# Kernel tuning notes

Hardware: AMD Instinct MI355X
Metric: run time of the kernel (lower is better)

Reference implementation:

```python
import jax, jax.numpy as jnp
import numpy as np

B, S, D, H = 4, 2048, 1024, 16
DK = D // H


def setup_inputs() -> dict:
    key = jax.random.key(0)
    ks = jax.random.split(key, 7)
    s = 1.0 / np.sqrt(D)
    return {
        "q": jax.random.normal(ks[0], (B, S, D), jnp.float32),
        "k": jax.random.normal(ks[1], (B, S, D), jnp.float32),
        "v": jax.random.normal(ks[2], (B, S, D), jnp.float32),
        "Wq": jax.random.normal(ks[3], (D, D), jnp.float32) * s,
        "Wk": jax.random.normal(ks[4], (D, D), jnp.float32) * s,
        "Wv": jax.random.normal(ks[5], (D, D), jnp.float32) * s,
        "Wo": jax.random.normal(ks[6], (D, D), jnp.float32) * s,
    }


def _split(x):
    # [B,S,D] -> [B,H,S,DK]
    return x.reshape(B, S, H, DK).transpose(0, 2, 1, 3)


def reference(q, k, v, Wq, Wk, Wv, Wo):
    # Linear projections (nn.Linear with bias=False: x @ W^T)
    qh = _split(q @ Wq.T)
    kh = _split(k @ Wk.T)
    vh = _split(v @ Wv.T)
    scale = 1.0 / jnp.sqrt(jnp.asarray(DK, qh.dtype))
    # attention scores [B,H,S,S]
    attn = jnp.einsum("bhqd,bhkd->bhqk", qh, kh) * scale
    # causal mask: disallow k > q
    causal = jnp.tril(jnp.ones((S, S), dtype=bool))
    attn = jnp.where(causal[None, None], attn, -jnp.inf)
    attn = jax.nn.softmax(attn, axis=-1)  # dropout p=0.0 -> identity
    out = jnp.einsum("bhqk,bhkd->bhqd", attn, vh)
    # combine heads [B,H,S,DK] -> [B,S,D]
    out = out.transpose(0, 2, 1, 3).reshape(B, S, D)
    return out @ Wo.T
```

## Files before the change

kernel.cpp:

```cpp
#include <hip/hip_runtime.h>
#include <math.h>
#include <stdint.h>

#define B_  4
#define S_  2048
#define D_  1024
#define H_  16
#define DK_ 64
#define NR_ (B_ * S_)

typedef _Float16 half8  __attribute__((ext_vector_type(8)));
typedef _Float16 half4  __attribute__((ext_vector_type(4)));
typedef float    floatx4 __attribute__((ext_vector_type(4)));

__global__ __launch_bounds__(256)
void split_f32(const float* __restrict__ src, _Float16* __restrict__ hi,
               _Float16* __restrict__ lo, int n8) {
    const int i = blockIdx.x * 256 + threadIdx.x;
    if (i >= n8) return;
    const float4* s4 = (const float4*)src;
    float4 a = s4[2 * i];
    float4 b = s4[2 * i + 1];
    float f[8] = {a.x, a.y, a.z, a.w, b.x, b.y, b.z, b.w};
    union { half8 v; _Float16 h[8]; } H, L;
    #pragma unroll
    for (int j = 0; j < 8; ++j) {
        _Float16 h = (_Float16)f[j];
        H.h[j] = h;
        L.h[j] = (_Float16)(f[j] - (float)h);
    }
    *(half8*)(hi + (size_t)i * 8) = H.v;
    *(half8*)(lo + (size_t)i * 8) = L.v;
}

__global__ __launch_bounds__(256)
void split_w4(const float* __restrict__ w0, const float* __restrict__ w1,
              const float* __restrict__ w2, const float* __restrict__ w3,
              _Float16* __restrict__ wbase, int n8) {
    const int i = blockIdx.x * 256 + threadIdx.x;
    if (i >= n8) return;
    const float* src = (blockIdx.y == 0) ? w0 : (blockIdx.y == 1) ? w1 :
                       (blockIdx.y == 2) ? w2 : w3;
    _Float16* hi = wbase + (size_t)blockIdx.y * 2 * ((size_t)D_ * D_);
    _Float16* lo = hi + (size_t)D_ * D_;
    const float4* s4 = (const float4*)src;
    float4 a = s4[2 * i];
    float4 b = s4[2 * i + 1];
    float f[8] = {a.x, a.y, a.z, a.w, b.x, b.y, b.z, b.w};
    union { half8 v; _Float16 h[8]; } H, L;
    #pragma unroll
    for (int j = 0; j < 8; ++j) {
        _Float16 h = (_Float16)f[j];
        H.h[j] = h;
        L.h[j] = (_Float16)(f[j] - (float)h);
    }
    *(half8*)(hi + (size_t)i * 8) = H.v;
    *(half8*)(lo + (size_t)i * 8) = L.v;
}

#define GBN 128
#define GBM 128
#define GBK 32
#define LDH 40

__global__ __launch_bounds__(256, 3)
void gemm_xwt_mfma(const _Float16* __restrict__ Xh, const _Float16* __restrict__ Xl,
                   const _Float16* __restrict__ Wh, const _Float16* __restrict__ Wl,
                   void* __restrict__ out0, int mode) {
    __shared__ __align__(16) _Float16 Whi[GBM][LDH];
    __shared__ __align__(16) _Float16 Wlo[GBM][LDH];
    const int K = D_;

    const int tid  = threadIdx.x;
    const int wave = tid >> 6;
    const int lane = tid & 63;
    const int row16 = lane & 15;
    const int quad  = lane >> 4;
    const int n0 = blockIdx.x * GBN;
    const int m0 = blockIdx.y * GBM;

    const int wrow = tid >> 1;
    const int wc   = (tid & 1) << 4;

    const _Float16* aHb = Xh + (size_t)(n0 + wave * 32 + row16) * K + quad * 8;
    const _Float16* aLb = Xl + (size_t)(n0 + wave * 32 + row16) * K + quad * 8;

    floatx4 acc[2][8];
    const floatx4 zero4 = {0.f, 0.f, 0.f, 0.f};
    #pragma unroll
    for (int i = 0; i < 2; ++i)
        #pragma unroll
        for (int j = 0; j < 8; ++j) acc[i][j] = zero4;

    half8 pa_h0, pa_h1, pa_l0, pa_l1;
    uint4 wh0, wh1, wl0, wl1;
    auto load_regs = [&](int k0) {
        pa_h0 = *(const half8*)(aHb + k0);
        pa_h1 = *(const half8*)(aHb + (size_t)16 * K + k0);
        pa_l0 = *(const half8*)(aLb + k0);
        pa_l1 = *(const half8*)(aLb + (size_t)16 * K + k0);
        const _Float16* pwh = Wh + (size_t)(m0 + wrow) * K + k0 + wc;
        const _Float16* pwl = Wl + (size_t)(m0 + wrow) * K + k0 + wc;
        wh0 = *(const uint4*)pwh;
        wh1 = *(const uint4*)(pwh + 8);
        wl0 = *(const uint4*)pwl;
        wl1 = *(const uint4*)(pwl + 8);
    };

    load_regs(0);
    for (int k0 = 0; k0 < K; k0 += GBK) {
        half8 a_hi[2] = {pa_h0, pa_h1};
        half8 a_lo[2] = {pa_l0, pa_l1};
        __syncthreads();
        *(uint4*)&Whi[wrow][wc]     = wh0;
        *(uint4*)&Whi[wrow][wc + 8] = wh1;
        *(uint4*)&Wlo[wrow][wc]     = wl0;
        *(uint4*)&Wlo[wrow][wc + 8] = wl1;
        __syncthreads();
        if (k0 + GBK < K) load_regs(k0 + GBK);

        #pragma unroll
        for (int mj = 0; mj < 8; ++mj) {
            const int r = mj * 16 + row16;
            half8 b_hi = *(const half8*)&Whi[r][quad * 8];
            half8 b_lo = *(const half8*)&Wlo[r][quad * 8];
            #pragma unroll
            for (int ni = 0; ni < 2; ++ni) {
                acc[ni][mj] = __builtin_amdgcn_mfma_f32_16x16x32_f16(
                    a_hi[ni], b_hi, acc[ni][mj], 0, 0, 0);
                acc[ni][mj] = __builtin_amdgcn_mfma_f32_16x16x32_f16(
                    a_hi[ni], b_lo, acc[ni][mj], 0, 0, 0);
                acc[ni][mj] = __builtin_amdgcn_mfma_f32_16x16x32_f16(
                    a_lo[ni], b_hi, acc[ni][mj], 0, 0, 0);
            }
        }
    }

    #pragma unroll
    for (int ni = 0; ni < 2; ++ni)
        #pragma unroll
        for (int mj = 0; mj < 8; ++mj) {
            if (mode == 2) {
                const int s  = n0 + wave * 32 + ni * 16 + quad * 4;
                const int b  = s >> 11;
                const int sr = s & (S_ - 1);
                const int m  = m0 + mj * 16 + row16;
                const int h  = m >> 6;
                const int dk = m & 63;
                half4 h4;
                #pragma unroll
                for (int r = 0; r < 4; ++r) h4[r] = (_Float16)acc[ni][mj][r];
                *(half4*)((_Float16*)out0 +
                          (((size_t)b * H_ + h) * DK_ + dk) * S_ + sr) = h4;
            } else {
                #pragma unroll
                for (int rg = 0; rg < 4; ++rg) {
                    const int n = n0 + wave * 32 + ni * 16 + quad * 4 + rg;
                    const int m = m0 + mj * 16 + row16;
                    const float v = acc[ni][mj][rg];
                    if (mode == 0) {
                        ((float*)out0)[(size_t)n * D_ + m] = v;
                    } else {
                        const int b  = n >> 11;
                        const int s  = n & (S_ - 1);
                        const int h  = m >> 6;
                        const int dk = m & 63;
                        union { _Float16 h16; uint16_t u; } hi, lo;
                        hi.h16 = (_Float16)v;
                        lo.h16 = (_Float16)(v - (float)hi.h16);
                        uint32_t u = ((uint32_t)lo.u << 16) | (uint32_t)hi.u;
                        ((uint32_t*)out0)[(((size_t)b * H_ + h) * S_ + s) * DK_ + dk] = u;
                    }
                }
            }
        }
}

__global__ __launch_bounds__(256)
void attn_mfma(const uint32_t* __restrict__ Qhl, const uint32_t* __restrict__ Khl,
               const _Float16* __restrict__ Vth,
               _Float16* __restrict__ Ahi, _Float16* __restrict__ Alo) {
    __shared__ __align__(16) _Float16 KhiC[64][64];
    __shared__ __align__(16) _Float16 KloC[64][64];
    __shared__ __align__(16) _Float16 VC[64][64];
    __shared__ __align__(16) _Float16 PCT[4][16][72];

    const int bh = blockIdx.y;
    const int qt = (int)(gridDim.x - 1) - (int)blockIdx.x;
    const int q0 = qt * 64;
    const int tid  = threadIdx.x;
    const int wave = tid >> 6;
    const int lane = tid & 63;
    const int c    = lane & 15;
    const int quad = lane >> 4;

    const uint32_t* Kb = Khl + (size_t)bh * S_ * DK_;
    const _Float16* Vb = Vth + (size_t)bh * DK_ * S_;

    half8 qhi[2], qlo[2];
    {
        const uint32_t* Qrow = Qhl + ((size_t)bh * S_ + q0 + wave * 16 + c) * DK_;
        #pragma unroll
        for (int ks = 0; ks < 2; ++ks) {
            uint32_t u[8];
            *(uint4*)&u[0] = *(const uint4*)(Qrow + ks * 32 + quad * 8);
            *(uint4*)&u[4] = *(const uint4*)(Qrow + ks * 32 + quad * 8 + 4);
            union { half8 v; uint16_t s[8]; } hi, lo;
            #pragma unroll
            for (int j = 0; j < 8; ++j) {
                hi.s[j] = (uint16_t)(u[j] & 0xffffu);
                lo.s[j] = (uint16_t)(u[j] >> 16);
            }
            qhi[ks] = hi.v; qlo[ks] = lo.v;
        }
    }

    floatx4 acc_o[4];
    const floatx4 zero4 = {0.f, 0.f, 0.f, 0.f};
    #pragma unroll
    for (int dt = 0; dt < 4; ++dt) acc_o[dt] = zero4;
    float mrun = -INFINITY, lrun = 0.f;

    const int srow = tid >> 2;
    const int soff = (tid & 3) * 16;
    const int ch0  = (tid & 3) * 2;

    uint4 ku[4];
    uint4 vv[2];
    auto load_tile = [&](int kt) {
        const uint4* ksrc = (const uint4*)(Kb + (size_t)(kt * 64 + srow) * DK_ + soff);
        ku[0] = ksrc[0]; ku[1] = ksrc[1]; ku[2] = ksrc[2]; ku[3] = ksrc[3];
        const uint4* vsrc = (const uint4*)(Vb + (size_t)srow * S_ + kt * 64 + soff);
        vv[0] = vsrc[0]; vv[1] = vsrc[1];
    };
    auto write_tile = [&]() {
        #pragma unroll
        for (int hf = 0; hf < 2; ++hf) {
            const int swz = ((ch0 + hf) ^ (srow & 7)) * 8;
            uint32_t uu[8];
            *(uint4*)&uu[0] = ku[2 * hf];
            *(uint4*)&uu[4] = ku[2 * hf + 1];
            union { half8 v; uint16_t s[8]; } hi, lo;
            #pragma unroll
            for (int j = 0; j < 8; ++j) {
                hi.s[j] = (uint16_t)(uu[j] & 0xffffu);
                lo.s[j] = (uint16_t)(uu[j] >> 16);
            }
            *(half8*)&KhiC[srow][swz] = hi.v;
            *(half8*)&KloC[srow][swz] = lo.v;
            *(uint4*)&VC[srow][swz]   = vv[hf];
        }
    };

    const int qmy = q0 + wave * 16 + c;
    const floatx4 neg4 = {-INFINITY, -INFINITY, -INFINITY, -INFINITY};

    load_tile(0);
    write_tile();

    for (int kt = 0; kt <= qt; ++kt) {
        const int k0 = kt * 64;
        const bool diag = (kt == qt);
        __syncthreads();
        if (kt < qt) load_tile(kt + 1);

        floatx4 sc[4];
        #pragma unroll
        for (int t = 0; t < 4; ++t) {
            if (diag && t > wave) { sc[t] = neg4; continue; }
            floatx4 s4 = zero4;
            const int krow = t * 16 + c;
            #pragma unroll
            for (int ks = 0; ks < 2; ++ks) {
                const int swz = ((ks * 4 + quad) ^ (krow & 7)) * 8;
                half8 kb = *(const half8*)&KhiC[krow][swz];
                half8 kl = *(const half8*)&KloC[krow][swz];
                s4 = __builtin_amdgcn_mfma_f32_16x16x32_f16(kb, qhi[ks], s4, 0, 0, 0);
                s4 = __builtin_amdgcn_mfma_f32_16x16x32_f16(kl, qhi[ks], s4, 0, 0, 0);
                s4 = __builtin_amdgcn_mfma_f32_16x16x32_f16(kb, qlo[ks], s4, 0, 0, 0);
            }
            #pragma unroll
            for (int r = 0; r < 4; ++r) s4[r] *= 0.125f;
            if (diag && t == wave) {
                #pragma unroll
                for (int r = 0; r < 4; ++r) {
                    const int k = k0 + t * 16 + quad * 4 + r;
                    if (k > qmy) s4[r] = -INFINITY;
                }
            }
            sc[t] = s4;
        }

        float mx = -INFINITY;
        #pragma unroll
        for (int t = 0; t < 4; ++t)
            #pragma unroll
            for (int r = 0; r < 4; ++r) mx = fmaxf(mx, sc[t][r]);
        mx = fmaxf(mx, __shfl_xor(mx, 16));
        mx = fmaxf(mx, __shfl_xor(mx, 32));
        const float mnew  = fmaxf(mrun, mx);
        const float alpha = __expf(mrun - mnew);
        float ls = 0.f;
        #pragma unroll
        for (int t = 0; t < 4; ++t) {
            half4 p4;
            #pragma unroll
            for (int r = 0; r < 4; ++r) {
                const float p = __expf(sc[t][r] - mnew);
                ls += p;
                p4[r] = (_Float16)p;
            }
            *(half4*)&PCT[wave][c][t * 16 + quad * 4] = p4;
        }
        lrun = alpha * lrun + ls;
        mrun = mnew;
        #pragma unroll
        for (int dt = 0; dt < 4; ++dt)
            #pragma unroll
            for (int r = 0; r < 4; ++r) acc_o[dt][r] *= alpha;

        #pragma unroll
        for (int kc = 0; kc < 2; ++kc) {
            if (diag && kc == 1 && wave < 2) continue;
            half8 pb = *(const half8*)&PCT[wave][c][kc * 32 + quad * 8];
            #pragma unroll
            for (int dt = 0; dt < 4; ++dt) {
                const int vrow = dt * 16 + c;
                const int swz = ((kc * 4 + quad) ^ (vrow & 7)) * 8;
                half8 va = *(const half8*)&VC[vrow][swz];
                acc_o[dt] = __builtin_amdgcn_mfma_f32_16x16x32_f16(va, pb, acc_o[dt], 0, 0, 0);
            }
        }

        __syncthreads();
        if (kt < qt) write_tile();
    }

    float l = lrun;
    l += __shfl_xor(l, 16);
    l += __shfl_xor(l, 32);
    const float inv = 1.f / l;
    const int b = bh >> 4, h = bh & 15;
    _Float16* dh = Ahi + ((size_t)b * S_ + qmy) * D_ + h * DK_;
    _Float16* dl = Alo + ((size_t)b * S_ + qmy) * D_ + h * DK_;
    #pragma unroll
    for (int dt = 0; dt < 4; ++dt) {
        half4 hh, ll;
        #pragma unroll
        for (int r = 0; r < 4; ++r) {
            const float o = acc_o[dt][r] * inv;
            hh[r] = (_Float16)o;
            ll[r] = (_Float16)(o - (float)hh[r]);
        }
        *(half4*)(dh + dt * 16 + quad * 4) = hh;
        *(half4*)(dl + dt * 16 + quad * 4) = ll;
    }
}

extern "C" void kernel_launch(void* const* d_in, const int* in_sizes, int n_in,
                              void* d_out, int out_size, void* d_ws, size_t ws_size,
                              hipStream_t stream) {
    const float* q  = (const float*)d_in[0];
    const float* k  = (const float*)d_in[1];
    const float* v  = (const float*)d_in[2];
    const float* Wq = (const float*)d_in[3];
    const float* Wk = (const float*)d_in[4];
    const float* Wv = (const float*)d_in[5];
    const float* Wo = (const float*)d_in[6];
    float* out = (float*)d_out;

    const size_t SZ  = (size_t)B_ * S_ * D_;
    const size_t WSZ = (size_t)D_ * D_;

    _Float16* ws    = (_Float16*)d_ws;
    _Float16* xhi   = ws;
    _Float16* xlo   = xhi + SZ;
    _Float16* wbase = xlo + SZ;
    uint32_t* Qhl = (uint32_t*)(wbase + 8 * WSZ);
    uint32_t* Khl = (uint32_t*)(wbase + 8 * WSZ + 2 * SZ);
    _Float16* Vth = wbase + 8 * WSZ + 4 * SZ;
    _Float16* Ahi = xhi;
    _Float16* Alo = xlo;

    _Float16* wq_hi = wbase + 0 * 2 * WSZ, *wq_lo = wq_hi + WSZ;
    _Float16* wk_hi = wbase + 1 * 2 * WSZ, *wk_lo = wk_hi + WSZ;
    _Float16* wv_hi = wbase + 2 * 2 * WSZ, *wv_lo = wv_hi + WSZ;
    _Float16* wo_hi = wbase + 3 * 2 * WSZ, *wo_lo = wo_hi + WSZ;

    const int nx8 = (int)(SZ / 8);
    const int nw8 = (int)(WSZ / 8);
    dim3 gb(NR_ / GBN, D_ / GBM);
    dim3 ga(S_ / 64, B_ * H_);
    dim3 gw(nw8 / 256, 4);

    split_w4<<<gw, 256, 0, stream>>>(Wq, Wk, Wv, Wo, wbase, nw8);

    split_f32<<<nx8 / 256, 256, 0, stream>>>(q, xhi, xlo, nx8);
    gemm_xwt_mfma<<<gb, 256, 0, stream>>>(xhi, xlo, wq_hi, wq_lo, Qhl, 1);

    split_f32<<<nx8 / 256, 256, 0, stream>>>(k, xhi, xlo, nx8);
    gemm_xwt_mfma<<<gb, 256, 0, stream>>>(xhi, xlo, wk_hi, wk_lo, Khl, 1);

    split_f32<<<nx8 / 256, 256, 0, stream>>>(v, xhi, xlo, nx8);
    gemm_xwt_mfma<<<gb, 256, 0, stream>>>(xhi, xlo, wv_hi, wv_lo, Vth, 2);

    attn_mfma<<<ga, 256, 0, stream>>>(Qhl, Khl, Vth, Ahi, Alo);

    gemm_xwt_mfma<<<gb, 256, 0, stream>>>(Ahi, Alo, wo_hi, wo_lo, out, 0);
}
```

Before: 616.2 us.

## Double GEMM K-tile and pass attention output as packed hi/lo pairs

Raises the GEMM K tile from 32 to 64 with matching LDS padding, so each tile does two MFMA sub-steps per barrier pair and the loop has half as many iterations and syncs. The attention kernel now writes its output as interleaved hi/lo fp16 pairs in 32-bit words. The output-projection GEMM reads these through a new packed-A mode and unpacks them in registers. The larger prefetch buffers raise register pressure under the 3-blocks-per-SM launch bound, and the unpacking adds ALU work.

```diff
diff --git a/kernel.cpp b/kernel.cpp
--- a/kernel.cpp
+++ b/kernel.cpp
@@ -60,13 +60,13 @@
 
 #define GBN 128
 #define GBM 128
-#define GBK 32
-#define LDH 40
+#define GBK 64
+#define LDH 72
 
 __global__ __launch_bounds__(256, 3)
 void gemm_xwt_mfma(const _Float16* __restrict__ Xh, const _Float16* __restrict__ Xl,
                    const _Float16* __restrict__ Wh, const _Float16* __restrict__ Wl,
-                   void* __restrict__ out0, int mode) {
+                   void* __restrict__ out0, int mode, int apack) {
     __shared__ __align__(16) _Float16 Whi[GBM][LDH];
     __shared__ __align__(16) _Float16 Wlo[GBM][LDH];
     const int K = D_;
@@ -80,10 +80,11 @@
     const int m0 = blockIdx.y * GBM;
 
     const int wrow = tid >> 1;
-    const int wc   = (tid & 1) << 4;
+    const int wc   = (tid & 1) << 5;
 
     const _Float16* aHb = Xh + (size_t)(n0 + wave * 32 + row16) * K + quad * 8;
     const _Float16* aLb = Xl + (size_t)(n0 + wave * 32 + row16) * K + quad * 8;
+    const uint32_t* aPb = (const uint32_t*)Xh + (size_t)(n0 + wave * 32 + row16) * K + quad * 8;
 
     floatx4 acc[2][8];
     const floatx4 zero4 = {0.f, 0.f, 0.f, 0.f};
@@ -92,48 +93,81 @@
         #pragma unroll
         for (int j = 0; j < 8; ++j) acc[i][j] = zero4;
 
-    half8 pa_h0, pa_h1, pa_l0, pa_l1;
-    uint4 wh0, wh1, wl0, wl1;
+    half8 pa_h[2][2], pa_l[2][2];
+    uint4 wh[4], wl[4];
     auto load_regs = [&](int k0) {
-        pa_h0 = *(const half8*)(aHb + k0);
-        pa_h1 = *(const half8*)(aHb + (size_t)16 * K + k0);
-        pa_l0 = *(const half8*)(aLb + k0);
-        pa_l1 = *(const half8*)(aLb + (size_t)16 * K + k0);
+        if (apack) {
+            #pragma unroll
+            for (int ni = 0; ni < 2; ++ni)
+                #pragma unroll
+                for (int ks = 0; ks < 2; ++ks) {
+                    const uint32_t* p = aPb + (size_t)ni * 16 * K + k0 + ks * 32;
+                    uint32_t u[8];
+                    *(uint4*)&u[0] = *(const uint4*)p;
+                    *(uint4*)&u[4] = *(const uint4*)(p + 4);
+                    union { half8 v; uint16_t s[8]; } hi, lo;
+                    #pragma unroll
+                    for (int j = 0; j < 8; ++j) {
+                        hi.s[j] = (uint16_t)(u[j] & 0xffffu);
+                        lo.s[j] = (uint16_t)(u[j] >> 16);
+                    }
+                    pa_h[ni][ks] = hi.v;
+                    pa_l[ni][ks] = lo.v;
+                }
+        } else {
+            #pragma unroll
+            for (int ni = 0; ni < 2; ++ni)
+                #pragma unroll
+                for (int ks = 0; ks < 2; ++ks) {
+                    pa_h[ni][ks] = *(const half8*)(aHb + (size_t)ni * 16 * K + k0 + ks * 32);
+                    pa_l[ni][ks] = *(const half8*)(aLb + (size_t)ni * 16 * K + k0 + ks * 32);
+                }
+        }
         const _Float16* pwh = Wh + (size_t)(m0 + wrow) * K + k0 + wc;
         const _Float16* pwl = Wl + (size_t)(m0 + wrow) * K + k0 + wc;
-        wh0 = *(const uint4*)pwh;
-        wh1 = *(const uint4*)(pwh + 8);
-        wl0 = *(const uint4*)pwl;
-        wl1 = *(const uint4*)(pwl + 8);
+        #pragma unroll
+        for (int c = 0; c < 4; ++c) {
+            wh[c] = *(const uint4*)(pwh + c * 8);
+            wl[c] = *(const uint4*)(pwl + c * 8);
+        }
     };
 
     load_regs(0);
     for (int k0 = 0; k0 < K; k0 += GBK) {
-        half8 a_hi[2] = {pa_h0, pa_h1};
-        half8 a_lo[2] = {pa_l0, pa_l1};
+        half8 a_hi[2][2], a_lo[2][2];
+        #pragma unroll
+        for (int ni = 0; ni < 2; ++ni)
+            #pragma unroll
+            for (int ks = 0; ks < 2; ++ks) {
+                a_hi[ni][ks] = pa_h[ni][ks];
+                a_lo[ni][ks] = pa_l[ni][ks];
+            }
         __syncthreads();
-        *(uint4*)&Whi[wrow][wc]     = wh0;
-        *(uint4*)&Whi[wrow][wc + 8] = wh1;
-        *(uint4*)&Wlo[wrow][wc]     = wl0;
-        *(uint4*)&Wlo[wrow][wc + 8] = wl1;
+        #pragma unroll
+        for (int c = 0; c < 4; ++c) {
+            *(uint4*)&Whi[wrow][wc + c * 8] = wh[c];
+            *(uint4*)&Wlo[wrow][wc + c * 8] = wl[c];
+        }
         __syncthreads();
         if (k0 + GBK < K) load_regs(k0 + GBK);
 
         #pragma unroll
-        for (int mj = 0; mj < 8; ++mj) {
-            const int r = mj * 16 + row16;
-            half8 b_hi = *(const half8*)&Whi[r][quad * 8];
-            half8 b_lo = *(const half8*)&Wlo[r][quad * 8];
-            #pragma unroll
-            for (int ni = 0; ni < 2; ++ni) {
-                acc[ni][mj] = __builtin_amdgcn_mfma_f32_16x16x32_f16(
-                    a_hi[ni], b_hi, acc[ni][mj], 0, 0, 0);
-                acc[ni][mj] = __builtin_amdgcn_mfma_f32_16x16x32_f16(
-                    a_hi[ni], b_lo, acc[ni][mj], 0, 0, 0);
-                acc[ni][mj] = __builtin_amdgcn_mfma_f32_16x16x32_f16(
-                    a_lo[ni], b_hi, acc[ni][mj], 0, 0, 0);
-            }
-        }
+        for (int ks = 0; ks < 2; ++ks)
+            #pragma unroll
+            for (int mj = 0; mj < 8; ++mj) {
+                const int r = mj * 16 + row16;
+                half8 b_hi = *(const half8*)&Whi[r][ks * 32 + quad * 8];
+                half8 b_lo = *(const half8*)&Wlo[r][ks * 32 + quad * 8];
+                #pragma unroll
+                for (int ni = 0; ni < 2; ++ni) {
+                    acc[ni][mj] = __builtin_amdgcn_mfma_f32_16x16x32_f16(
+                        a_hi[ni][ks], b_hi, acc[ni][mj], 0, 0, 0);
+                    acc[ni][mj] = __builtin_amdgcn_mfma_f32_16x16x32_f16(
+                        a_hi[ni][ks], b_lo, acc[ni][mj], 0, 0, 0);
+                    acc[ni][mj] = __builtin_amdgcn_mfma_f32_16x16x32_f16(
+                        a_lo[ni][ks], b_hi, acc[ni][mj], 0, 0, 0);
+                }
+            }
     }
 
     #pragma unroll
@@ -178,8 +212,7 @@
 
 __global__ __launch_bounds__(256)
 void attn_mfma(const uint32_t* __restrict__ Qhl, const uint32_t* __restrict__ Khl,
-               const _Float16* __restrict__ Vth,
-               _Float16* __restrict__ Ahi, _Float16* __restrict__ Alo) {
+               const _Float16* __restrict__ Vth, uint32_t* __restrict__ Ahl) {
     __shared__ __align__(16) _Float16 KhiC[64][64];
     __shared__ __align__(16) _Float16 KloC[64][64];
     __shared__ __align__(16) _Float16 VC[64][64];
@@ -341,19 +374,19 @@
     l += __shfl_xor(l, 32);
     const float inv = 1.f / l;
     const int b = bh >> 4, h = bh & 15;
-    _Float16* dh = Ahi + ((size_t)b * S_ + qmy) * D_ + h * DK_;
-    _Float16* dl = Alo + ((size_t)b * S_ + qmy) * D_ + h * DK_;
+    uint32_t* dstA = Ahl + ((size_t)b * S_ + qmy) * D_ + h * DK_;
     #pragma unroll
     for (int dt = 0; dt < 4; ++dt) {
-        half4 hh, ll;
+        uint4 pk;
         #pragma unroll
         for (int r = 0; r < 4; ++r) {
             const float o = acc_o[dt][r] * inv;
-            hh[r] = (_Float16)o;
-            ll[r] = (_Float16)(o - (float)hh[r]);
-        }
-        *(half4*)(dh + dt * 16 + quad * 4) = hh;
-        *(half4*)(dl + dt * 16 + quad * 4) = ll;
+            union { _Float16 h16; uint16_t u; } hi, lo;
+            hi.h16 = (_Float16)o;
+            lo.h16 = (_Float16)(o - (float)hi.h16);
+            ((uint32_t*)&pk)[r] = ((uint32_t)lo.u << 16) | (uint32_t)hi.u;
+        }
+        *(uint4*)(dstA + dt * 16 + quad * 4) = pk;
     }
 }
 
@@ -379,8 +412,7 @@
     uint32_t* Qhl = (uint32_t*)(wbase + 8 * WSZ);
     uint32_t* Khl = (uint32_t*)(wbase + 8 * WSZ + 2 * SZ);
     _Float16* Vth = wbase + 8 * WSZ + 4 * SZ;
-    _Float16* Ahi = xhi;
-    _Float16* Alo = xlo;
+    uint32_t* Ahl = (uint32_t*)xhi;
 
     _Float16* wq_hi = wbase + 0 * 2 * WSZ, *wq_lo = wq_hi + WSZ;
     _Float16* wk_hi = wbase + 1 * 2 * WSZ, *wk_lo = wk_hi + WSZ;
@@ -396,15 +428,16 @@
     split_w4<<<gw, 256, 0, stream>>>(Wq, Wk, Wv, Wo, wbase, nw8);
 
     split_f32<<<nx8 / 256, 256, 0, stream>>>(q, xhi, xlo, nx8);
-    gemm_xwt_mfma<<<gb, 256, 0, stream>>>(xhi, xlo, wq_hi, wq_lo, Qhl, 1);
+    gemm_xwt_mfma<<<gb, 256, 0, stream>>>(xhi, xlo, wq_hi, wq_lo, Qhl, 1, 0);
 
     split_f32<<<nx8 / 256, 256, 0, stream>>>(k, xhi, xlo, nx8);
-    gemm_xwt_mfma<<<gb, 256, 0, stream>>>(xhi, xlo, wk_hi, wk_lo, Khl, 1);
+    gemm_xwt_mfma<<<gb, 256, 0, stream>>>(xhi, xlo, wk_hi, wk_lo, Khl, 1, 0);
 
     split_f32<<<nx8 / 256, 256, 0, stream>>>(v, xhi, xlo, nx8);
-    gemm_xwt_mfma<<<gb, 256, 0, stream>>>(xhi, xlo, wv_hi, wv_lo, Vth, 2);
-
-    attn_mfma<<<ga, 256, 0, stream>>>(Qhl, Khl, Vth, Ahi, Alo);
-
-    gemm_xwt_mfma<<<gb, 256, 0, stream>>>(Ahi, Alo, wo_hi, wo_lo, out, 0);
+    gemm_xwt_mfma<<<gb, 256, 0, stream>>>(xhi, xlo, wv_hi, wv_lo, Vth, 2, 0);
+
+    attn_mfma<<<ga, 256, 0, stream>>>(Qhl, Khl, Vth, Ahl);
+
+    gemm_xwt_mfma<<<gb, 256, 0, stream>>>((const _Float16*)Ahl, nullptr,
+                                          wo_hi, wo_lo, out, 0, 1);
 }
```

Result: slower. 897.9 us (+45.7%).

## Fuse fp32 hi/lo split into projection GEMM loads and pack attention output

Applied to the files above, without the earlier changes.

Removes the three standalone split_f32 kernels: the projection GEMM now loads fp32 activations directly and splits them into fp16 hi/lo in registers. The attention output is written as packed 32-bit hi|lo pairs into its own buffer, and the output projection unpacks them on load. This cuts kernel launches and the intermediate write and read of the split activation buffers. In exchange, the GEMM A-operand loads are twice as wide and the conversion math is repeated by every column block that rereads the same rows.

```diff
diff --git a/kernel.cpp b/kernel.cpp
--- a/kernel.cpp
+++ b/kernel.cpp
@@ -12,26 +12,6 @@
 typedef _Float16 half8  __attribute__((ext_vector_type(8)));
 typedef _Float16 half4  __attribute__((ext_vector_type(4)));
 typedef float    floatx4 __attribute__((ext_vector_type(4)));
-
-__global__ __launch_bounds__(256)
-void split_f32(const float* __restrict__ src, _Float16* __restrict__ hi,
-               _Float16* __restrict__ lo, int n8) {
-    const int i = blockIdx.x * 256 + threadIdx.x;
-    if (i >= n8) return;
-    const float4* s4 = (const float4*)src;
-    float4 a = s4[2 * i];
-    float4 b = s4[2 * i + 1];
-    float f[8] = {a.x, a.y, a.z, a.w, b.x, b.y, b.z, b.w};
-    union { half8 v; _Float16 h[8]; } H, L;
-    #pragma unroll
-    for (int j = 0; j < 8; ++j) {
-        _Float16 h = (_Float16)f[j];
-        H.h[j] = h;
-        L.h[j] = (_Float16)(f[j] - (float)h);
-    }
-    *(half8*)(hi + (size_t)i * 8) = H.v;
-    *(half8*)(lo + (size_t)i * 8) = L.v;
-}
 
 __global__ __launch_bounds__(256)
 void split_w4(const float* __restrict__ w0, const float* __restrict__ w1,
@@ -63,8 +43,9 @@
 #define GBK 32
 #define LDH 40
 
+template <int APACK>
 __global__ __launch_bounds__(256, 3)
-void gemm_xwt_mfma(const _Float16* __restrict__ Xh, const _Float16* __restrict__ Xl,
+void gemm_xwt_mfma(const void* __restrict__ Xin,
                    const _Float16* __restrict__ Wh, const _Float16* __restrict__ Wl,
                    void* __restrict__ out0, int mode) {
     __shared__ __align__(16) _Float16 Whi[GBM][LDH];
@@ -82,8 +63,10 @@
     const int wrow = tid >> 1;
     const int wc   = (tid & 1) << 4;
 
-    const _Float16* aHb = Xh + (size_t)(n0 + wave * 32 + row16) * K + quad * 8;
-    const _Float16* aLb = Xl + (size_t)(n0 + wave * 32 + row16) * K + quad * 8;
+    const float*    aFb = (const float*)Xin +
+                          (size_t)(n0 + wave * 32 + row16) * K + quad * 8;
+    const uint32_t* aPb = (const uint32_t*)Xin +
+                          (size_t)(n0 + wave * 32 + row16) * K + quad * 8;
 
     floatx4 acc[2][8];
     const floatx4 zero4 = {0.f, 0.f, 0.f, 0.f};
@@ -92,13 +75,40 @@
         #pragma unroll
         for (int j = 0; j < 8; ++j) acc[i][j] = zero4;
 
-    half8 pa_h0, pa_h1, pa_l0, pa_l1;
+    half8 pa_h[2], pa_l[2];
     uint4 wh0, wh1, wl0, wl1;
     auto load_regs = [&](int k0) {
-        pa_h0 = *(const half8*)(aHb + k0);
-        pa_h1 = *(const half8*)(aHb + (size_t)16 * K + k0);
-        pa_l0 = *(const half8*)(aLb + k0);
-        pa_l1 = *(const half8*)(aLb + (size_t)16 * K + k0);
+        #pragma unroll
+        for (int ni = 0; ni < 2; ++ni) {
+            if (APACK == 0) {
+                const float* p = aFb + (size_t)ni * 16 * K + k0;
+                float4 f0 = *(const float4*)p;
+                float4 f1 = *(const float4*)(p + 4);
+                float f[8] = {f0.x, f0.y, f0.z, f0.w, f1.x, f1.y, f1.z, f1.w};
+                union { half8 v; _Float16 h[8]; } hi, lo;
+                #pragma unroll
+                for (int j = 0; j < 8; ++j) {
+                    _Float16 h = (_Float16)f[j];
+                    hi.h[j] = h;
+                    lo.h[j] = (_Float16)(f[j] - (float)h);
+                }
+                pa_h[ni] = hi.v;
+                pa_l[ni] = lo.v;
+            } else {
+                const uint32_t* p = aPb + (size_t)ni * 16 * K + k0;
+                uint32_t u[8];
+                *(uint4*)&u[0] = *(const uint4*)p;
+                *(uint4*)&u[4] = *(const uint4*)(p + 4);
+                union { half8 v; uint16_t s[8]; } hi, lo;
+                #pragma unroll
+                for (int j = 0; j < 8; ++j) {
+                    hi.s[j] = (uint16_t)(u[j] & 0xffffu);
+                    lo.s[j] = (uint16_t)(u[j] >> 16);
+                }
+                pa_h[ni] = hi.v;
+                pa_l[ni] = lo.v;
+            }
+        }
         const _Float16* pwh = Wh + (size_t)(m0 + wrow) * K + k0 + wc;
         const _Float16* pwl = Wl + (size_t)(m0 + wrow) * K + k0 + wc;
         wh0 = *(const uint4*)pwh;
@@ -109,8 +119,8 @@
 
     load_regs(0);
     for (int k0 = 0; k0 < K; k0 += GBK) {
-        half8 a_hi[2] = {pa_h0, pa_h1};
-        half8 a_lo[2] = {pa_l0, pa_l1};
+        half8 a_hi[2] = {pa_h[0], pa_h[1]};
+        half8 a_lo[2] = {pa_l[0], pa_l[1]};
         __syncthreads();
         *(uint4*)&Whi[wrow][wc]     = wh0;
         *(uint4*)&Whi[wrow][wc + 8] = wh1;
@@ -178,8 +188,7 @@
 
 __global__ __launch_bounds__(256)
 void attn_mfma(const uint32_t* __restrict__ Qhl, const uint32_t* __restrict__ Khl,
-               const _Float16* __restrict__ Vth,
-               _Float16* __restrict__ Ahi, _Float16* __restrict__ Alo) {
+               const _Float16* __restrict__ Vth, uint32_t* __restrict__ Ahl) {
     __shared__ __align__(16) _Float16 KhiC[64][64];
     __shared__ __align__(16) _Float16 KloC[64][64];
     __shared__ __align__(16) _Float16 VC[64][64];
@@ -341,19 +350,19 @@
     l += __shfl_xor(l, 32);
     const float inv = 1.f / l;
     const int b = bh >> 4, h = bh & 15;
-    _Float16* dh = Ahi + ((size_t)b * S_ + qmy) * D_ + h * DK_;
-    _Float16* dl = Alo + ((size_t)b * S_ + qmy) * D_ + h * DK_;
+    uint32_t* dstA = Ahl + ((size_t)b * S_ + qmy) * D_ + h * DK_;
     #pragma unroll
     for (int dt = 0; dt < 4; ++dt) {
-        half4 hh, ll;
+        uint4 pk;
         #pragma unroll
         for (int r = 0; r < 4; ++r) {
             const float o = acc_o[dt][r] * inv;
-            hh[r] = (_Float16)o;
-            ll[r] = (_Float16)(o - (float)hh[r]);
-        }
-        *(half4*)(dh + dt * 16 + quad * 4) = hh;
-        *(half4*)(dl + dt * 16 + quad * 4) = ll;
+            union { _Float16 h16; uint16_t u; } hi, lo;
+            hi.h16 = (_Float16)o;
+            lo.h16 = (_Float16)(o - (float)hi.h16);
+            ((uint32_t*)&pk)[r] = ((uint32_t)lo.u << 16) | (uint32_t)hi.u;
+        }
+        *(uint4*)(dstA + dt * 16 + quad * 4) = pk;
     }
 }
 
@@ -373,21 +382,17 @@
     const size_t WSZ = (size_t)D_ * D_;
 
     _Float16* ws    = (_Float16*)d_ws;
-    _Float16* xhi   = ws;
-    _Float16* xlo   = xhi + SZ;
-    _Float16* wbase = xlo + SZ;
+    _Float16* wbase = ws;
     uint32_t* Qhl = (uint32_t*)(wbase + 8 * WSZ);
     uint32_t* Khl = (uint32_t*)(wbase + 8 * WSZ + 2 * SZ);
     _Float16* Vth = wbase + 8 * WSZ + 4 * SZ;
-    _Float16* Ahi = xhi;
-    _Float16* Alo = xlo;
+    uint32_t* Ahl = (uint32_t*)(wbase + 8 * WSZ + 5 * SZ);
 
     _Float16* wq_hi = wbase + 0 * 2 * WSZ, *wq_lo = wq_hi + WSZ;
     _Float16* wk_hi = wbase + 1 * 2 * WSZ, *wk_lo = wk_hi + WSZ;
     _Float16* wv_hi = wbase + 2 * 2 * WSZ, *wv_lo = wv_hi + WSZ;
     _Float16* wo_hi = wbase + 3 * 2 * WSZ, *wo_lo = wo_hi + WSZ;
 
-    const int nx8 = (int)(SZ / 8);
     const int nw8 = (int)(WSZ / 8);
     dim3 gb(NR_ / GBN, D_ / GBM);
     dim3 ga(S_ / 64, B_ * H_);
@@ -395,16 +400,11 @@
 
     split_w4<<<gw, 256, 0, stream>>>(Wq, Wk, Wv, Wo, wbase, nw8);
 
-    split_f32<<<nx8 / 256, 256, 0, stream>>>(q, xhi, xlo, nx8);
-    gemm_xwt_mfma<<<gb, 256, 0, stream>>>(xhi, xlo, wq_hi, wq_lo, Qhl, 1);
-
-    split_f32<<<nx8 / 256, 256, 0, stream>>>(k, xhi, xlo, nx8);
-    gemm_xwt_mfma<<<gb, 256, 0, stream>>>(xhi, xlo, wk_hi, wk_lo, Khl, 1);
-
-    split_f32<<<nx8 / 256, 256, 0, stream>>>(v, xhi, xlo, nx8);
-    gemm_xwt_mfma<<<gb, 256, 0, stream>>>(xhi, xlo, wv_hi, wv_lo, Vth, 2);
-
-    attn_mfma<<<ga, 256, 0, stream>>>(Qhl, Khl, Vth, Ahi, Alo);
-
-    gemm_xwt_mfma<<<gb, 256, 0, stream>>>(Ahi, Alo, wo_hi, wo_lo, out, 0);
+    gemm_xwt_mfma<0><<<gb, 256, 0, stream>>>(q, wq_hi, wq_lo, Qhl, 1);
+    gemm_xwt_mfma<0><<<gb, 256, 0, stream>>>(k, wk_hi, wk_lo, Khl, 1);
+    gemm_xwt_mfma<0><<<gb, 256, 0, stream>>>(v, wv_hi, wv_lo, Vth, 2);
+
+    attn_mfma<<<ga, 256, 0, stream>>>(Qhl, Khl, Vth, Ahl);
+
+    gemm_xwt_mfma<1><<<gb, 256, 0, stream>>>(Ahl, wo_hi, wo_lo, out, 0);
 }
```

New measurement: 578.7 us. -6.1%, faster.
